# Kernel optimization log

Hardware: AMD Instinct MI355X
Metric: run time of the kernel (lower is better)

Reference implementation:

```python
import jax, jax.numpy as jnp
import numpy as np

C = 512
NH = 4
HD = C // NH
G = 32  # min(32, C) and C % 32 == 0
EPS = 1e-5


def setup_inputs() -> dict:
    key = jax.random.key(0)
    ks = jax.random.split(key, 11)
    s = 1.0 / np.sqrt(C)
    return {
        "x": jax.random.normal(ks[0], (16, C, 32, 32), dtype=jnp.float32),
        "gamma": jnp.ones((C,), jnp.float32),
        "beta": jnp.zeros((C,), jnp.float32),
        "wq": jax.random.normal(ks[1], (C, C), jnp.float32) * s,
        "bq": jax.random.normal(ks[2], (C,), jnp.float32) * 0.01,
        "wk": jax.random.normal(ks[3], (C, C), jnp.float32) * s,
        "bk": jax.random.normal(ks[4], (C,), jnp.float32) * 0.01,
        "wv": jax.random.normal(ks[5], (C, C), jnp.float32) * s,
        "bv": jax.random.normal(ks[6], (C,), jnp.float32) * 0.01,
        "wp": jax.random.normal(ks[7], (C, C), jnp.float32) * s,
        "bp": jax.random.normal(ks[8], (C,), jnp.float32) * 0.01,
    }


def _group_norm(x, gamma, beta):
    b, c, h, w = x.shape
    xr = x.reshape(b, G, c // G, h, w)
    mean = xr.mean(axis=(2, 3, 4), keepdims=True)
    var = xr.var(axis=(2, 3, 4), keepdims=True)
    xn = ((xr - mean) * jax.lax.rsqrt(var + EPS)).reshape(b, c, h, w)
    return xn * gamma[None, :, None, None] + beta[None, :, None, None]


def _conv1x1(x, w, b):
    # 1x1 conv == per-position channel GEMM
    return jnp.einsum('oc,bchw->bohw', w, x) + b[None, :, None, None]


def reference(x, gamma, beta, wq, bq, wk, bk, wv, bv, wp, bp):
    b, c, h, w = x.shape
    hw = h * w
    scale = HD ** (-0.5)
    hn = _group_norm(x, gamma, beta)
    q = _conv1x1(hn, wq, bq).reshape(b, NH, HD, hw)
    k = _conv1x1(hn, wk, bk).reshape(b, NH, HD, hw)
    v = _conv1x1(hn, wv, bv).reshape(b, NH, HD, hw)
    attn = jnp.einsum('bhdq,bhdk->bhqk', q, k) * scale  # [b, nh, hw, hw]
    attn = jax.nn.softmax(attn, axis=-1)
    out = jnp.einsum('bhqk,bhdk->bhdq', attn, v)  # [b, nh, hd, hw]
    out = out.reshape(b, c, h, w)
    out = _conv1x1(out, wp, bp)
    return x + out
```

## Files before the change

kernel.cpp:

```cpp
#include <hip/hip_runtime.h>
#include <math.h>

#define CCH 512
#define NH 4
#define HD 128
#define HW 1024
#define BATCH 16
#define EPS 1e-5f

typedef __attribute__((ext_vector_type(8))) short bfrag;
typedef __attribute__((ext_vector_type(4))) float f4;
typedef __attribute__((ext_vector_type(16))) float f16v;

static __device__ __forceinline__ unsigned short f2bf(float f) {
  union { float f; unsigned u; } v;
  v.f = f;
  unsigned r = v.u + 0x7fff + ((v.u >> 16) & 1);
  return (unsigned short)(r >> 16);
}
static __device__ __forceinline__ unsigned pack2(unsigned short a, unsigned short b) {
  return (unsigned)a | ((unsigned)b << 16);
}
static __device__ __forceinline__ unsigned cvt_pk_bf16(float a, float b) {
  unsigned r;
  asm("v_cvt_pk_bf16_f32 %0, %1, %2" : "=v"(r) : "v"(a), "v"(b));
  return r;
}
#if defined(__has_builtin) && __has_builtin(__builtin_amdgcn_exp2f)
#define EXP2(x) __builtin_amdgcn_exp2f(x)
#else
#define EXP2(x) __expf((x) * 0.6931471805599453f)
#endif
static __device__ __forceinline__ void ldg_lds16(const unsigned short* g,
                                                 unsigned short* l) {
  __builtin_amdgcn_global_load_lds(
      (const __attribute__((address_space(1))) unsigned int*)g,
      (__attribute__((address_space(3))) unsigned int*)l, 16, 0, 0);
}

#define QSCALE (0.08838834764831845f * 1.4426950408889634f)

__global__ __launch_bounds__(256) void wcvt_kernel(const float* __restrict__ s0,
                                                   const float* __restrict__ s1,
                                                   const float* __restrict__ s2,
                                                   const float* __restrict__ s3,
                                                   unsigned short* __restrict__ d) {
  const float* srcs[4] = {s0, s1, s2, s3};
  const float* s = srcs[blockIdx.y];
  unsigned short* dp = d + (size_t)blockIdx.y * CCH * CCH;
  int i = blockIdx.x * 256 + threadIdx.x;
  f4 v = ((const f4*)s)[i];
  ushort4 o;
  o.x = f2bf(v.x); o.y = f2bf(v.y); o.z = f2bf(v.z); o.w = f2bf(v.w);
  ((ushort4*)dp)[i] = o;
}

__global__ __launch_bounds__(256) void gn_kernel(const float* __restrict__ x,
                                                 const float* __restrict__ gamma,
                                                 const float* __restrict__ beta,
                                                 unsigned short* __restrict__ hn) {
  int b = blockIdx.x >> 5, g = blockIdx.x & 31;
  const float* xp = x + ((size_t)b * CCH + g * 16) * HW;
  int t = threadIdx.x;
  float s = 0.f, ss = 0.f;
  const f4* xp4 = (const f4*)xp;
  for (int i = t; i < 4096; i += 256) {
    f4 v = xp4[i];
    s += v.x + v.y + v.z + v.w;
    ss += v.x * v.x + v.y * v.y + v.z * v.z + v.w * v.w;
  }
#pragma unroll
  for (int off = 32; off > 0; off >>= 1) {
    s += __shfl_xor(s, off);
    ss += __shfl_xor(ss, off);
  }
  __shared__ float rs[4], rss[4];
  int w = t >> 6;
  if ((t & 63) == 0) { rs[w] = s; rss[w] = ss; }
  __syncthreads();
  s = rs[0] + rs[1] + rs[2] + rs[3];
  ss = rss[0] + rss[1] + rss[2] + rss[3];
  const float invn = 1.f / (16 * HW);
  float mean = s * invn;
  float var = ss * invn - mean * mean;
  float rstd = rsqrtf(var + EPS);
  float a_[16], b_[16];
#pragma unroll
  for (int c = 0; c < 16; ++c) {
    float gm = gamma[g * 16 + c] * rstd;
    a_[c] = gm;
    b_[c] = beta[g * 16 + c] - mean * gm;
  }
#pragma unroll
  for (int i = 0; i < 4; ++i) {
    int p = t + 256 * i;
    unsigned short tv[16];
#pragma unroll
    for (int c = 0; c < 16; ++c) tv[c] = f2bf(xp[c * HW + p] * a_[c] + b_[c]);
    uint4 u0, u1;
    u0.x = pack2(tv[0], tv[1]);  u0.y = pack2(tv[2], tv[3]);
    u0.z = pack2(tv[4], tv[5]);  u0.w = pack2(tv[6], tv[7]);
    u1.x = pack2(tv[8], tv[9]);  u1.y = pack2(tv[10], tv[11]);
    u1.z = pack2(tv[12], tv[13]); u1.w = pack2(tv[14], tv[15]);
    unsigned short* dst = hn + ((size_t)b * HW + p) * CCH + g * 16;
    *(uint4*)dst = u0;
    *(uint4*)(dst + 8) = u1;
  }
}

template <int PROJ>
__global__ __launch_bounds__(256, 3) void mm_kernel(
    const unsigned short* __restrict__ Xt, const unsigned short* __restrict__ Wb,
    const float* __restrict__ b0, const float* __restrict__ b1,
    const float* __restrict__ b2, const float* __restrict__ resid,
    unsigned short* __restrict__ O0, unsigned short* __restrict__ O1,
    unsigned short* __restrict__ O2, float* __restrict__ Ofp) {
  int b = blockIdx.z;
  int p0 = blockIdx.x * 128;
  int c0g = blockIdx.y * 128;
  __shared__ __align__(16) unsigned short Xs[128 * 32];
  __shared__ __align__(16) unsigned short Ws[128 * 32];
  int t = threadIdx.x;
  int w = t >> 6, lane = t & 63, l15 = lane & 15, quad = lane >> 4;
  int wp = (w & 1) * 64, wc = (w >> 1) * 64;
  const unsigned short* Xb = Xt + (size_t)b * HW * CCH;
  const unsigned short* Wr = Wb + (size_t)c0g * CCH;
  f4 acc[4][4] = {};
  for (int k0 = 0; k0 < CCH; k0 += 32) {
    __syncthreads();
#pragma unroll
    for (int j = 0; j < 2; ++j) {
      int chk = w * 2 + j;
      int r = chk * 16 + (lane >> 2);
      int c = (lane & 3) ^ (r & 3);
      ldg_lds16(&Xb[(size_t)(p0 + r) * CCH + k0 + c * 8], &Xs[chk * 512]);
      ldg_lds16(&Wr[(size_t)r * CCH + k0 + c * 8], &Ws[chk * 512]);
    }
    __syncthreads();
    bfrag af[4], bf[4];
#pragma unroll
    for (int pt = 0; pt < 4; ++pt) {
      int r = wp + pt * 16 + l15;
      af[pt] = *(const bfrag*)&Xs[r * 32 + (quad ^ (r & 3)) * 8];
    }
#pragma unroll
    for (int ct = 0; ct < 4; ++ct) {
      int r = wc + ct * 16 + l15;
      bf[ct] = *(const bfrag*)&Ws[r * 32 + (quad ^ (r & 3)) * 8];
    }
#pragma unroll
    for (int pt = 0; pt < 4; ++pt)
#pragma unroll
      for (int ct = 0; ct < 4; ++ct)
        acc[pt][ct] = __builtin_amdgcn_mfma_f32_16x16x32_bf16(
            af[pt], bf[ct], acc[pt][ct], 0, 0, 0);
  }
  if (PROJ) {
#pragma unroll
    for (int ct = 0; ct < 4; ++ct) {
      int ch = c0g + wc + ct * 16 + l15;
      float bi = b0[ch];
#pragma unroll
      for (int pt = 0; pt < 4; ++pt) {
        int pos = p0 + wp + pt * 16 + quad * 4;
        f4 v = acc[pt][ct];
        size_t off = (size_t)b * CCH * HW + (size_t)ch * HW + pos;
        float4 rv = *(const float4*)&resid[off];
        float4 st;
        st.x = v.x + bi + rv.x; st.y = v.y + bi + rv.y;
        st.z = v.z + bi + rv.z; st.w = v.w + bi + rv.w;
        *(float4*)&Ofp[off] = st;
      }
    }
  } else {
    int mat = c0g >> 9;
    int c0 = c0g & 511;
    const float* bias = mat == 0 ? b0 : (mat == 1 ? b1 : b2);
    unsigned short* O = mat == 0 ? O0 : (mat == 1 ? O1 : O2);
    const float sc = (mat == 0) ? QSCALE : 1.0f;
#pragma unroll
    for (int ct = 0; ct < 4; ++ct) {
      int ch = c0 + wc + ct * 16 + l15;
      float bi = bias[ch];
#pragma unroll
      for (int pt = 0; pt < 4; ++pt) {
        int pos = p0 + wp + pt * 16 + quad * 4;
        f4 v = acc[pt][ct];
        if (mat < 2) {
          unsigned short* Op = O + (size_t)b * HW * CCH;
          Op[(size_t)(pos + 0) * CCH + ch] = f2bf((v.x + bi) * sc);
          Op[(size_t)(pos + 1) * CCH + ch] = f2bf((v.y + bi) * sc);
          Op[(size_t)(pos + 2) * CCH + ch] = f2bf((v.z + bi) * sc);
          Op[(size_t)(pos + 3) * CCH + ch] = f2bf((v.w + bi) * sc);
        } else {
          unsigned short* Op = O + (size_t)b * CCH * HW;
          ushort4 st;
          st.x = f2bf(v.x + bi); st.y = f2bf(v.y + bi);
          st.z = f2bf(v.z + bi); st.w = f2bf(v.w + bi);
          *(ushort4*)&Op[(size_t)ch * HW + pos] = st;
        }
      }
    }
  }
}

__global__ __launch_bounds__(256, 2) void attn_kernel(
    const unsigned short* __restrict__ Qt, const unsigned short* __restrict__ Kt,
    const unsigned short* __restrict__ Vc, unsigned short* __restrict__ Ot) {
  int bh = blockIdx.x;
  int b = bh >> 2, h = bh & 3;
  int q0 = blockIdx.y * 128;
  int t = threadIdx.x;
  int w = t >> 6, lane = t & 63;
  int l31 = lane & 31, half = lane >> 5;
  __shared__ __align__(16) unsigned short Ks[2][64 * 128];
  __shared__ __align__(16) unsigned short Vs[2][128 * 64];
  int q = q0 + w * 32 + l31;
  const unsigned short* Kbase = Kt + (size_t)b * HW * CCH + h * HD;
  const unsigned short* Vbase = Vc + ((size_t)b * CCH + h * HD) * HW;
  bfrag qf[8];
#pragma unroll
  for (int ks = 0; ks < 8; ++ks)
    qf[ks] = *(const bfrag*)&Qt[((size_t)b * HW + q) * CCH + h * HD +
                                ks * 16 + half * 8];
  f16v o[4] = {};
  float ls[4] = {};
  auto stage = [&](int kt, int bi) {
    int kk0 = kt * 64;
#pragma unroll
    for (int j = 0; j < 4; ++j) {
      int chk = w * 4 + j;
      {
        int r = chk * 4 + (lane >> 4);
        int c = (lane & 15) ^ (r & 15);
        ldg_lds16(&Kbase[(size_t)(kk0 + r) * CCH + c * 8], &Ks[bi][chk * 512]);
      }
      {
        int r = chk * 8 + (lane >> 3);
        int c = (lane & 7) ^ (r & 7);
        ldg_lds16(&Vbase[(size_t)r * HW + kk0 + c * 8], &Vs[bi][chk * 512]);
      }
    }
  };
  stage(0, 0);
  for (int kt = 0; kt < 16; ++kt) {
    __syncthreads();
    if (kt < 15) stage(kt + 1, (kt + 1) & 1);
    const unsigned short* K_ = Ks[kt & 1];
    const unsigned short* V_ = Vs[kt & 1];
    f16v S[2] = {};
    __builtin_amdgcn_s_setprio(1);
#pragma unroll
    for (int ks = 0; ks < 8; ++ks) {
      int c16 = ks * 2 + half;
#pragma unroll
      for (int mt = 0; mt < 2; ++mt) {
        int r = mt * 32 + l31;
        bfrag kf = *(const bfrag*)&K_[r * 128 + ((c16 ^ (r & 15)) << 3)];
        S[mt] = __builtin_amdgcn_mfma_f32_32x32x16_bf16(kf, qf[ks], S[mt],
                                                        0, 0, 0);
      }
    }
    __builtin_amdgcn_s_setprio(0);
    unsigned pd[16];
#pragma unroll
    for (int mt = 0; mt < 2; ++mt)
#pragma unroll
      for (int i = 0; i < 8; ++i) {
        float p0 = EXP2(S[mt][2 * i]);
        float p1 = EXP2(S[mt][2 * i + 1]);
        ls[i & 3] += p0 + p1;
        pd[mt * 8 + i] = cvt_pk_bf16(p0, p1);
      }
#pragma unroll
    for (int mt = 0; mt < 2; ++mt)
#pragma unroll
      for (int s = 0; s < 2; ++s) {
        int base = mt * 8 + s * 4;
        unsigned s0 = half ? pd[base + 0] : pd[base + 2];
        unsigned s1 = half ? pd[base + 1] : pd[base + 3];
        unsigned r0 = (unsigned)__shfl_xor((int)s0, 32);
        unsigned r1 = (unsigned)__shfl_xor((int)s1, 32);
        union { unsigned u[4]; bfrag f; } pf;
        pf.u[0] = half ? r0 : pd[base + 0];
        pf.u[1] = half ? r1 : pd[base + 1];
        pf.u[2] = half ? pd[base + 2] : r0;
        pf.u[3] = half ? pd[base + 3] : r1;
        int c8 = (mt * 2 + s) * 2 + half;
        __builtin_amdgcn_s_setprio(1);
#pragma unroll
        for (int dt = 0; dt < 4; ++dt) {
          int r = dt * 32 + l31;
          bfrag vf = *(const bfrag*)&V_[r * 64 + ((c8 ^ (r & 7)) << 3)];
          o[dt] = __builtin_amdgcn_mfma_f32_32x32x16_bf16(vf, pf.f, o[dt],
                                                          0, 0, 0);
        }
        __builtin_amdgcn_s_setprio(0);
      }
  }
  float lrow = (ls[0] + ls[1]) + (ls[2] + ls[3]);
  lrow += __shfl_xor(lrow, 32);
  float inv = 1.f / lrow;
  unsigned short* Op = Ot + ((size_t)b * HW + q) * CCH + h * HD;
#pragma unroll
  for (int dt = 0; dt < 4; ++dt)
#pragma unroll
    for (int rg = 0; rg < 4; ++rg) {
      int d = dt * 32 + rg * 8 + half * 4;
      uint2 st;
      st.x = cvt_pk_bf16(o[dt][rg * 4 + 0] * inv, o[dt][rg * 4 + 1] * inv);
      st.y = cvt_pk_bf16(o[dt][rg * 4 + 2] * inv, o[dt][rg * 4 + 3] * inv);
      *(uint2*)&Op[d] = st;
    }
}

extern "C" void kernel_launch(void* const* d_in, const int* in_sizes, int n_in,
                              void* d_out, int out_size, void* d_ws,
                              size_t ws_size, hipStream_t stream) {
  const float* x = (const float*)d_in[0];
  const float* gamma = (const float*)d_in[1];
  const float* beta = (const float*)d_in[2];
  const float* wq = (const float*)d_in[3];
  const float* bq = (const float*)d_in[4];
  const float* wk = (const float*)d_in[5];
  const float* bk = (const float*)d_in[6];
  const float* wv = (const float*)d_in[7];
  const float* bv = (const float*)d_in[8];
  const float* wp = (const float*)d_in[9];
  const float* bp = (const float*)d_in[10];

  const size_t TS = (size_t)BATCH * HW * CCH;
  unsigned short* wB = (unsigned short*)d_ws;
  unsigned short* hn = wB + (size_t)4 * CCH * CCH;
  unsigned short* Qt = hn + TS;
  unsigned short* Kt = Qt + TS;
  unsigned short* Vc = Kt + TS;
  unsigned short* Ot = hn;

  wcvt_kernel<<<dim3(256, 4), 256, 0, stream>>>(wq, wk, wv, wp, wB);
  gn_kernel<<<dim3(BATCH * 32), 256, 0, stream>>>(x, gamma, beta, hn);
  mm_kernel<0><<<dim3(8, 12, BATCH), 256, 0, stream>>>(
      hn, wB, bq, bk, bv, nullptr, Qt, Kt, Vc, nullptr);
  attn_kernel<<<dim3(64, 8), 256, 0, stream>>>(Qt, Kt, Vc, Ot);
  mm_kernel<1><<<dim3(8, 4, BATCH), 256, 0, stream>>>(
      Ot, wB + (size_t)3 * CCH * CCH, bp, bp, bp, x, nullptr, nullptr, nullptr,
      (float*)d_out);
}
```

Baseline: 222.6 us.

## Double-buffer GEMM LDS tiles, cache GN loads in registers, use permlane32 swap

The 1x1-conv GEMM kernel now double-buffers its LDS tiles. The next K slice is prefetched while MFMAs run on the current one, and one barrier per iteration is used instead of two. Group norm keeps its 16 float4 loads in registers so x is read once instead of twice, and it converts with the packed bf16 instruction. The attention P-fragment exchange replaces shfl_xor plus selects with v_permlane32_swap. Together these raise LDS use per block and register pressure, which could reduce occupancy.

Result: faster. 211.4 us (-5.0%).

```diff
diff --git a/kernel.cpp b/kernel.cpp
--- a/kernel.cpp
+++ b/kernel.cpp
@@ -64,8 +64,11 @@
   int t = threadIdx.x;
   float s = 0.f, ss = 0.f;
   const f4* xp4 = (const f4*)xp;
-  for (int i = t; i < 4096; i += 256) {
-    f4 v = xp4[i];
+  f4 vv[16];
+#pragma unroll
+  for (int c = 0; c < 16; ++c) {
+    f4 v = xp4[c * 256 + t];
+    vv[c] = v;
     s += v.x + v.y + v.z + v.w;
     ss += v.x * v.x + v.y * v.y + v.z * v.z + v.w * v.w;
   }
@@ -93,15 +96,16 @@
   }
 #pragma unroll
   for (int i = 0; i < 4; ++i) {
-    int p = t + 256 * i;
-    unsigned short tv[16];
-#pragma unroll
-    for (int c = 0; c < 16; ++c) tv[c] = f2bf(xp[c * HW + p] * a_[c] + b_[c]);
+    int p = 4 * t + i;
     uint4 u0, u1;
-    u0.x = pack2(tv[0], tv[1]);  u0.y = pack2(tv[2], tv[3]);
-    u0.z = pack2(tv[4], tv[5]);  u0.w = pack2(tv[6], tv[7]);
-    u1.x = pack2(tv[8], tv[9]);  u1.y = pack2(tv[10], tv[11]);
-    u1.z = pack2(tv[12], tv[13]); u1.w = pack2(tv[14], tv[15]);
+    u0.x = cvt_pk_bf16(vv[0][i] * a_[0] + b_[0], vv[1][i] * a_[1] + b_[1]);
+    u0.y = cvt_pk_bf16(vv[2][i] * a_[2] + b_[2], vv[3][i] * a_[3] + b_[3]);
+    u0.z = cvt_pk_bf16(vv[4][i] * a_[4] + b_[4], vv[5][i] * a_[5] + b_[5]);
+    u0.w = cvt_pk_bf16(vv[6][i] * a_[6] + b_[6], vv[7][i] * a_[7] + b_[7]);
+    u1.x = cvt_pk_bf16(vv[8][i] * a_[8] + b_[8], vv[9][i] * a_[9] + b_[9]);
+    u1.y = cvt_pk_bf16(vv[10][i] * a_[10] + b_[10], vv[11][i] * a_[11] + b_[11]);
+    u1.z = cvt_pk_bf16(vv[12][i] * a_[12] + b_[12], vv[13][i] * a_[13] + b_[13]);
+    u1.w = cvt_pk_bf16(vv[14][i] * a_[14] + b_[14], vv[15][i] * a_[15] + b_[15]);
     unsigned short* dst = hn + ((size_t)b * HW + p) * CCH + g * 16;
     *(uint4*)dst = u0;
     *(uint4*)(dst + 8) = u1;
@@ -118,35 +122,38 @@
   int b = blockIdx.z;
   int p0 = blockIdx.x * 128;
   int c0g = blockIdx.y * 128;
-  __shared__ __align__(16) unsigned short Xs[128 * 32];
-  __shared__ __align__(16) unsigned short Ws[128 * 32];
+  __shared__ __align__(16) unsigned short Xs[2][4096];
+  __shared__ __align__(16) unsigned short Ws[2][4096];
   int t = threadIdx.x;
   int w = t >> 6, lane = t & 63, l15 = lane & 15, quad = lane >> 4;
   int wp = (w & 1) * 64, wc = (w >> 1) * 64;
   const unsigned short* Xb = Xt + (size_t)b * HW * CCH;
   const unsigned short* Wr = Wb + (size_t)c0g * CCH;
   f4 acc[4][4] = {};
-  for (int k0 = 0; k0 < CCH; k0 += 32) {
-    __syncthreads();
+  auto stage = [&](int k0, int bi) {
 #pragma unroll
     for (int j = 0; j < 2; ++j) {
       int chk = w * 2 + j;
       int r = chk * 16 + (lane >> 2);
       int c = (lane & 3) ^ (r & 3);
-      ldg_lds16(&Xb[(size_t)(p0 + r) * CCH + k0 + c * 8], &Xs[chk * 512]);
-      ldg_lds16(&Wr[(size_t)r * CCH + k0 + c * 8], &Ws[chk * 512]);
-    }
-    __syncthreads();
+      ldg_lds16(&Xb[(size_t)(p0 + r) * CCH + k0 + c * 8], &Xs[bi][chk * 512]);
+      ldg_lds16(&Wr[(size_t)r * CCH + k0 + c * 8], &Ws[bi][chk * 512]);
+    }
+  };
+  stage(0, 0);
+  __syncthreads();
+  for (int k0 = 0, cur = 0; k0 < CCH; k0 += 32, cur ^= 1) {
+    if (k0 + 32 < CCH) stage(k0 + 32, cur ^ 1);
     bfrag af[4], bf[4];
 #pragma unroll
     for (int pt = 0; pt < 4; ++pt) {
       int r = wp + pt * 16 + l15;
-      af[pt] = *(const bfrag*)&Xs[r * 32 + (quad ^ (r & 3)) * 8];
+      af[pt] = *(const bfrag*)&Xs[cur][r * 32 + (quad ^ (r & 3)) * 8];
     }
 #pragma unroll
     for (int ct = 0; ct < 4; ++ct) {
       int r = wc + ct * 16 + l15;
-      bf[ct] = *(const bfrag*)&Ws[r * 32 + (quad ^ (r & 3)) * 8];
+      bf[ct] = *(const bfrag*)&Ws[cur][r * 32 + (quad ^ (r & 3)) * 8];
     }
 #pragma unroll
     for (int pt = 0; pt < 4; ++pt)
@@ -154,6 +161,7 @@
       for (int ct = 0; ct < 4; ++ct)
         acc[pt][ct] = __builtin_amdgcn_mfma_f32_16x16x32_bf16(
             af[pt], bf[ct], acc[pt][ct], 0, 0, 0);
+    __syncthreads();
   }
   if (PROJ) {
 #pragma unroll
@@ -277,15 +285,12 @@
 #pragma unroll
       for (int s = 0; s < 2; ++s) {
         int base = mt * 8 + s * 4;
-        unsigned s0 = half ? pd[base + 0] : pd[base + 2];
-        unsigned s1 = half ? pd[base + 1] : pd[base + 3];
-        unsigned r0 = (unsigned)__shfl_xor((int)s0, 32);
-        unsigned r1 = (unsigned)__shfl_xor((int)s1, 32);
+        unsigned a0 = pd[base + 0], a1 = pd[base + 1];
+        unsigned c0 = pd[base + 2], c1 = pd[base + 3];
+        asm("v_permlane32_swap_b32 %0, %1" : "+v"(a0), "+v"(c0));
+        asm("v_permlane32_swap_b32 %0, %1" : "+v"(a1), "+v"(c1));
         union { unsigned u[4]; bfrag f; } pf;
-        pf.u[0] = half ? r0 : pd[base + 0];
-        pf.u[1] = half ? r1 : pd[base + 1];
-        pf.u[2] = half ? pd[base + 2] : r0;
-        pf.u[3] = half ? pd[base + 3] : r1;
+        pf.u[0] = a0; pf.u[1] = a1; pf.u[2] = c0; pf.u[3] = c1;
         int c8 = (mt * 2 + s) * 2 + half;
         __builtin_amdgcn_s_setprio(1);
 #pragma unroll
```
